# Performance work log

Measured on AMD Instinct MI355X. Metric: run time of the kernel, lower is better.

Reference implementation:

```python
import jax, jax.numpy as jnp
import numpy as np

B, N, C, H = 4, 1024, 768, 12
D = C // H  # head_dim = 64


def setup_inputs() -> dict:
    key = jax.random.key(0)
    ks = jax.random.split(key, 6)
    x = jax.random.normal(ks[0], (B, N, C), dtype=jnp.float32)
    W_qkv = jax.random.normal(ks[1], (C, 3 * C), dtype=jnp.float32) * (C ** -0.5)
    b_qkv = jnp.zeros((3 * C,), dtype=jnp.float32)
    scale = jnp.asarray(D ** -0.5, dtype=jnp.float32)       # learnable scalar in torch
    riem_scale = jnp.asarray(D ** -0.5, dtype=jnp.float32)  # learnable scalar in torch
    # 1x1 Conv2d(2H -> H) == channel-mixing matrix [H, 2H] + bias [H]
    W_conv = jax.random.normal(ks[2], (H, 2 * H), dtype=jnp.float32) * ((2 * H) ** -0.5)
    b_conv = jnp.zeros((H,), dtype=jnp.float32)
    W_proj = jax.random.normal(ks[3], (C, C), dtype=jnp.float32) * (C ** -0.5)
    b_proj = jnp.zeros((C,), dtype=jnp.float32)
    return dict(x=x, W_qkv=W_qkv, b_qkv=b_qkv, scale=scale, riem_scale=riem_scale,
                W_conv=W_conv, b_conv=b_conv, W_proj=W_proj, b_proj=b_proj)


def reference(x, W_qkv, b_qkv, scale, riem_scale, W_conv, b_conv, W_proj, b_proj):
    Bx, Nx, Cx = x.shape
    Hh = W_conv.shape[0]
    d = Cx // Hh
    # qkv projection -> [3, B, H, N, d]
    qkv = (x @ W_qkv + b_qkv).reshape(Bx, Nx, 3, Hh, d).transpose(2, 0, 3, 1, 4)
    q, k, v = qkv[0], qkv[1], qkv[2]
    # standard scaled dot-product scores [B, H, N, N]
    attn = jnp.einsum('bhnd,bhmd->bhnm', q, k) * scale
    # covariance-Frobenius (Riemannian) scores: center along feature dim, then
    # <q_c q_c^T, k_c k_c^T>_F = (q_c . k_c)^2 pairwise
    qc = q - q.mean(axis=-1, keepdims=True)
    kc = k - k.mean(axis=-1, keepdims=True)
    attn_riem = jnp.einsum('bhnd,bhmd->bhnm', qc, kc) ** 2 * riem_scale
    # concat along head/channel dim -> [B, 2H, N, N], then 1x1 conv channel mix
    cat = jnp.concatenate([attn, attn_riem], axis=1)
    mixed = jnp.einsum('bcnm,oc->bonm', cat, W_conv) + b_conv[None, :, None, None]
    attn_ = jax.nn.softmax(mixed, axis=-1)  # [B, H, N, N]
    out = jnp.einsum('bhnm,bhmd->bhnd', attn_, v)
    out = out.transpose(0, 2, 1, 3).reshape(Bx, Nx, Cx)
    return out @ W_proj + b_proj, attn_
```

## Files before the change

### kernel.cpp

```cpp
#include <hip/hip_runtime.h>
#include <cstddef>
#include <cstdint>

#define B_ 4
#define N_ 1024
#define C_ 768
#define H_ 12
#define D_ 64

typedef __attribute__((ext_vector_type(8))) short bf16x8;
typedef __attribute__((ext_vector_type(4))) short s16x4;
typedef __attribute__((ext_vector_type(4))) float f32x4;
typedef __attribute__((ext_vector_type(2))) float f32x2;

#define MFMA16(a_, b_, c_) __builtin_amdgcn_mfma_f32_16x16x32_bf16((a_), (b_), (c_), 0, 0, 0)
#define GLLDS16(gp_, lp_) __builtin_amdgcn_global_load_lds( \
    (const __attribute__((address_space(1))) unsigned int*)(gp_), \
    (__attribute__((address_space(3))) unsigned int*)(lp_), 16, 0, 0)

__device__ __forceinline__ unsigned short f2bf(float f) {
  unsigned int u = __float_as_uint(f);
  u += 0x7fffu + ((u >> 16) & 1u);
  return (unsigned short)(u >> 16);
}
__device__ __forceinline__ float bf2f(unsigned short b) {
  return __uint_as_float(((unsigned int)b) << 16);
}
__device__ __forceinline__ short f2h(float f) {
  _Float16 h = (_Float16)f;
  short s;
  __builtin_memcpy(&s, &h, 2);
  return s;
}
__device__ __forceinline__ float h2f(short s) {
  _Float16 h;
  __builtin_memcpy(&h, &s, 2);
  return (float)h;
}

__global__ __launch_bounds__(256) void k_prep(const float* __restrict__ x,
                                              short* __restrict__ xhi, short* __restrict__ xlo,
                                              const float* __restrict__ Wq,
                                              short* __restrict__ Wthi, short* __restrict__ Wtlo,
                                              const float* __restrict__ Wp,
                                              short* __restrict__ Wpthi, short* __restrict__ Wptlo) {
  __shared__ float tile[32][33];
  const int f = blockIdx.x;
  const int t = threadIdx.x;
  if (f < 1536) {
    const size_t i = ((size_t)f * 256 + t) * 8;
    float4 a = *reinterpret_cast<const float4*>(&x[i]);
    float4 b = *reinterpret_cast<const float4*>(&x[i + 4]);
    float v[8] = {a.x, a.y, a.z, a.w, b.x, b.y, b.z, b.w};
    bf16x8 hi, lo;
#pragma unroll
    for (int j = 0; j < 8; ++j) {
      unsigned short h = f2bf(v[j]);
      hi[j] = (short)h;
      lo[j] = (short)f2bf(v[j] - bf2f(h));
    }
    *reinterpret_cast<bf16x8*>(&xhi[i]) = hi;
    *reinterpret_cast<bf16x8*>(&xlo[i]) = lo;
    return;
  }
  const float* W;
  short *Thi, *Tlo;
  int Kd, Nn, bx, by;
  if (f < 3264) {
    const int local = f - 1536;
    W = Wq; Thi = Wthi; Tlo = Wtlo; Kd = 768; Nn = 2304;
    bx = local % 72; by = local / 72;
  } else {
    const int local = f - 3264;
    W = Wp; Thi = Wpthi; Tlo = Wptlo; Kd = 768; Nn = 768;
    bx = local % 24; by = local / 24;
  }
  const int k0 = by * 32, n0 = bx * 32;
  const int r = t >> 3, cq = (t & 7) * 4;
  float4 v = *reinterpret_cast<const float4*>(&W[(size_t)(k0 + r) * Nn + n0 + cq]);
  tile[r][cq + 0] = v.x; tile[r][cq + 1] = v.y;
  tile[r][cq + 2] = v.z; tile[r][cq + 3] = v.w;
  __syncthreads();
  const int nrow = t >> 3, kq = (t & 7) * 4;
  s16x4 hi, lo;
#pragma unroll
  for (int i = 0; i < 4; ++i) {
    float fv = tile[kq + i][nrow];
    unsigned short h = f2bf(fv);
    hi[i] = (short)h;
    lo[i] = (short)f2bf(fv - bf2f(h));
  }
  *reinterpret_cast<s16x4*>(&Thi[(size_t)(n0 + nrow) * Kd + k0 + kq]) = hi;
  *reinterpret_cast<s16x4*>(&Tlo[(size_t)(n0 + nrow) * Kd + k0 + kq]) = lo;
}

__global__ __launch_bounds__(256) void k_fold(const float* __restrict__ Wc,
                                              const float* __restrict__ scale_p,
                                              const float* __restrict__ riem_p,
                                              float* __restrict__ Wfold) {
  const int t = threadIdx.x;
  const float scale = scale_p[0], riem = riem_p[0];
  for (int i = t; i < 288; i += 256)
    Wfold[i] = Wc[i] * (((i % 24) < 12) ? scale : riem);
}

__global__ __launch_bounds__(256) void k_gemm(const short* __restrict__ Ahi,
                                              const short* __restrict__ Alo,
                                              const short* __restrict__ Bhi,
                                              const short* __restrict__ Blo,
                                              const float* __restrict__ bias,
                                              float* __restrict__ Cout,
                                              int M, int Nn, int Kd) {
  __shared__ __align__(16) short sA[2][128 * 32];
  __shared__ __align__(16) short sB[2][64 * 32];
  const int tid = threadIdx.x;
  const int wv = tid >> 6, l = tid & 63;
  const int lr = l & 15, lg = l >> 4;
  const int row0 = blockIdx.y * 128;
  const int col0 = blockIdx.x * 64;
  const int wr = (wv >> 1) * 64;
  const int wc = (wv & 1) * 32;
  const int ar = tid >> 2, ac = tid & 3;
  f32x4 acc[4][2];
#pragma unroll
  for (int i = 0; i < 4; ++i)
#pragma unroll
    for (int j = 0; j < 2; ++j) acc[i][j] = (f32x4){0.f, 0.f, 0.f, 0.f};

  for (int k0 = 0; k0 < Kd; k0 += 32) {
#pragma unroll
    for (int j = 0; j < 2; ++j) {
      const int row = j * 64 + ar;
      const int cc = ac ^ ((row >> 1) & 3);
      const size_t so = (size_t)(row0 + row) * Kd + k0 + cc * 8;
      GLLDS16(Ahi + so, &sA[0][(j * 256 + (wv << 6)) * 8]);
      GLLDS16(Alo + so, &sA[1][(j * 256 + (wv << 6)) * 8]);
    }
    {
      const int row = ar;
      const int cc = ac ^ ((row >> 1) & 3);
      const size_t so = (size_t)(col0 + row) * Kd + k0 + cc * 8;
      GLLDS16(Bhi + so, &sB[0][(wv << 6) * 8]);
      GLLDS16(Blo + so, &sB[1][(wv << 6) * 8]);
    }
    __syncthreads();
    bf16x8 afh[4], afl[4], bfh[2], bfl[2];
#pragma unroll
    for (int ti = 0; ti < 4; ++ti) {
      const int row = wr + ti * 16 + lr;
      const int pc = lg ^ ((row >> 1) & 3);
      afh[ti] = *reinterpret_cast<const bf16x8*>(&sA[0][row * 32 + pc * 8]);
      afl[ti] = *reinterpret_cast<const bf16x8*>(&sA[1][row * 32 + pc * 8]);
    }
#pragma unroll
    for (int tj = 0; tj < 2; ++tj) {
      const int row = wc + tj * 16 + lr;
      const int pc = lg ^ ((row >> 1) & 3);
      bfh[tj] = *reinterpret_cast<const bf16x8*>(&sB[0][row * 32 + pc * 8]);
      bfl[tj] = *reinterpret_cast<const bf16x8*>(&sB[1][row * 32 + pc * 8]);
    }
#pragma unroll
    for (int ti = 0; ti < 4; ++ti)
#pragma unroll
      for (int tj = 0; tj < 2; ++tj) {
        acc[ti][tj] = MFMA16(afh[ti], bfh[tj], acc[ti][tj]);
        acc[ti][tj] = MFMA16(afl[ti], bfh[tj], acc[ti][tj]);
        acc[ti][tj] = MFMA16(afh[ti], bfl[tj], acc[ti][tj]);
      }
    __syncthreads();
  }
#pragma unroll
  for (int ti = 0; ti < 4; ++ti)
#pragma unroll
    for (int tj = 0; tj < 2; ++tj) {
      const int col = col0 + wc + tj * 16 + lr;
      const float bb = bias[col];
#pragma unroll
      for (int r = 0; r < 4; ++r) {
        const int row = row0 + wr + ti * 16 + lg * 4 + r;
        Cout[(size_t)row * Nn + col] = acc[ti][tj][r] + bb;
      }
    }
}

__global__ __launch_bounds__(256) void k_gemm128(const short* __restrict__ Ahi,
                                                 const short* __restrict__ Alo,
                                                 const short* __restrict__ Bhi,
                                                 const short* __restrict__ Blo,
                                                 const float* __restrict__ bias,
                                                 float* __restrict__ Cout,
                                                 int M, int Nn, int Kd) {
  __shared__ __align__(16) short sA[2][128 * 32];
  __shared__ __align__(16) short sB[2][128 * 32];
  const int tid = threadIdx.x;
  const int wv = tid >> 6, l = tid & 63;
  const int lr = l & 15, lg = l >> 4;
  const int row0 = blockIdx.y * 128;
  const int col0 = blockIdx.x * 128;
  const int wr = (wv >> 1) * 64;
  const int wc = (wv & 1) * 64;
  const int ar = tid >> 2, ac = tid & 3;
  f32x4 acc[4][4];
#pragma unroll
  for (int i = 0; i < 4; ++i)
#pragma unroll
    for (int j = 0; j < 4; ++j) acc[i][j] = (f32x4){0.f, 0.f, 0.f, 0.f};

  for (int k0 = 0; k0 < Kd; k0 += 32) {
#pragma unroll
    for (int j = 0; j < 2; ++j) {
      const int row = j * 64 + ar;
      const int cc = ac ^ ((row >> 1) & 3);
      const size_t ao = (size_t)(row0 + row) * Kd + k0 + cc * 8;
      const size_t bo = (size_t)(col0 + row) * Kd + k0 + cc * 8;
      GLLDS16(Ahi + ao, &sA[0][(j * 256 + (wv << 6)) * 8]);
      GLLDS16(Alo + ao, &sA[1][(j * 256 + (wv << 6)) * 8]);
      GLLDS16(Bhi + bo, &sB[0][(j * 256 + (wv << 6)) * 8]);
      GLLDS16(Blo + bo, &sB[1][(j * 256 + (wv << 6)) * 8]);
    }
    __syncthreads();
    bf16x8 afh[4], afl[4], bfh[4], bfl[4];
#pragma unroll
    for (int ti = 0; ti < 4; ++ti) {
      const int row = wr + ti * 16 + lr;
      const int pc = lg ^ ((row >> 1) & 3);
      afh[ti] = *reinterpret_cast<const bf16x8*>(&sA[0][row * 32 + pc * 8]);
      afl[ti] = *reinterpret_cast<const bf16x8*>(&sA[1][row * 32 + pc * 8]);
    }
#pragma unroll
    for (int tj = 0; tj < 4; ++tj) {
      const int row = wc + tj * 16 + lr;
      const int pc = lg ^ ((row >> 1) & 3);
      bfh[tj] = *reinterpret_cast<const bf16x8*>(&sB[0][row * 32 + pc * 8]);
      bfl[tj] = *reinterpret_cast<const bf16x8*>(&sB[1][row * 32 + pc * 8]);
    }
#pragma unroll
    for (int ti = 0; ti < 4; ++ti)
#pragma unroll
      for (int tj = 0; tj < 4; ++tj) {
        acc[ti][tj] = MFMA16(afh[ti], bfh[tj], acc[ti][tj]);
        acc[ti][tj] = MFMA16(afl[ti], bfh[tj], acc[ti][tj]);
        acc[ti][tj] = MFMA16(afh[ti], bfl[tj], acc[ti][tj]);
      }
    __syncthreads();
  }
#pragma unroll
  for (int ti = 0; ti < 4; ++ti)
#pragma unroll
    for (int tj = 0; tj < 4; ++tj) {
      const int col = col0 + wc + tj * 16 + lr;
      const float bb = bias[col];
#pragma unroll
      for (int r = 0; r < 4; ++r) {
        const int row = row0 + wr + ti * 16 + lg * 4 + r;
        Cout[(size_t)row * Nn + col] = acc[ti][tj][r] + bb;
      }
    }
}

__global__ __launch_bounds__(256) void k_qkv_post(const float* __restrict__ qkvf,
                                                  short* __restrict__ Qhi, short* __restrict__ Qlo,
                                                  short* __restrict__ KChi, short* __restrict__ KClo,
                                                  short* __restrict__ Vt,
                                                  float* __restrict__ Qm, float* __restrict__ Km) {
  __shared__ unsigned short lvh[64][33];
  const int b = blockIdx.z, h = blockIdx.y, n0 = blockIdx.x * 32;
  const int t = threadIdx.x;
  const int row = t >> 3, d0 = (t & 7) * 8;
  const int n = n0 + row;
  const float* base = qkvf + ((size_t)(b * 1024 + n)) * 2304 + h * 64 + d0;
  const size_t qko = ((size_t)(b * H_ + h) * N_ + n) * D_ + d0;

#pragma unroll
  for (int part = 0; part < 2; ++part) {
    float4 a = *reinterpret_cast<const float4*>(base + part * 768);
    float4 c = *reinterpret_cast<const float4*>(base + part * 768 + 4);
    float v[8] = {a.x, a.y, a.z, a.w, c.x, c.y, c.z, c.w};
    float s = v[0] + v[1] + v[2] + v[3] + v[4] + v[5] + v[6] + v[7];
#pragma unroll
    for (int off = 1; off < 8; off <<= 1) s += __shfl_xor(s, off);
    const float mean = s * (1.0f / 64.0f);
    if ((t & 7) == 0) (part ? Km : Qm)[(size_t)(b * H_ + h) * N_ + n] = mean;
    const float sub = part ? mean : 0.0f;
    bf16x8 hi, lo;
#pragma unroll
    for (int j = 0; j < 8; ++j) {
      const float fv = v[j] - sub;
      unsigned short hh = f2bf(fv);
      hi[j] = (short)hh;
      lo[j] = (short)f2bf(fv - bf2f(hh));
    }
    *reinterpret_cast<bf16x8*>((part ? KChi : Qhi) + qko) = hi;
    *reinterpret_cast<bf16x8*>((part ? KClo : Qlo) + qko) = lo;
  }
  {
    float4 a = *reinterpret_cast<const float4*>(base + 1536);
    float4 c = *reinterpret_cast<const float4*>(base + 1536 + 4);
    float v[8] = {a.x, a.y, a.z, a.w, c.x, c.y, c.z, c.w};
#pragma unroll
    for (int j = 0; j < 8; ++j) lvh[d0 + j][row] = f2bf(v[j]);
  }
  __syncthreads();
  const int d = t >> 2, c = t & 3;
  bf16x8 vh;
#pragma unroll
  for (int i = 0; i < 8; ++i) vh[i] = (short)lvh[d][c * 8 + i];
  const size_t vo = ((size_t)(b * H_ + h) * D_ + d) * N_ + n0 + c * 8;
  *reinterpret_cast<bf16x8*>(Vt + vo) = vh;
}

__global__ __launch_bounds__(256, 2) void k_scores(
    const short* __restrict__ Qhi, const short* __restrict__ Qlo,
    const short* __restrict__ KChi, const short* __restrict__ KClo,
    const float* __restrict__ Qm, const float* __restrict__ Km,
    const float* __restrict__ Wfold, float* __restrict__ logits,
    float2* __restrict__ stats) {
  __shared__ __align__(16) short sCh[2][32 * 64];
  __shared__ __align__(16) short sCl[2][32 * 64];
  __shared__ float sQm[12][64];
  __shared__ float sKm[12][32];

  const int t = threadIdx.x;
  const int b = blockIdx.z;
  const int n0 = blockIdx.y * 64, m0 = blockIdx.x * 32;
  const int wv = t >> 6, l = t & 63;
  const int lr = l & 15, lg = l >> 4;
  const size_t bh0 = (size_t)b * H_;

  for (int i = t; i < 768; i += 256)
    sQm[i >> 6][i & 63] = Qm[(bh0 + (i >> 6)) * N_ + n0 + (i & 63)];
  for (int i = t; i < 384; i += 256)
    sKm[i >> 5][i & 31] = Km[(bh0 + (i >> 5)) * N_ + m0 + (i & 31)];

  const int srow = t >> 3;
  const int scs = (t & 7) ^ (srow & 7);
  const size_t csrc = (bh0 * N_ + m0 + srow) * D_ + scs * 8;
  const size_t hstep = (size_t)N_ * D_;
  const int nb = n0 + wv * 16;
  const size_t qsrc = (bh0 * N_ + nb + lr) * D_ + lg * 8;

  GLLDS16(KChi + csrc, &sCh[0][wv * 512]);
  GLLDS16(KClo + csrc, &sCl[0][wv * 512]);
  bf16x8 qh0 = *reinterpret_cast<const bf16x8*>(Qhi + qsrc);
  bf16x8 qh1 = *reinterpret_cast<const bf16x8*>(Qhi + qsrc + 32);
  bf16x8 ql0 = *reinterpret_cast<const bf16x8*>(Qlo + qsrc);
  bf16x8 ql1 = *reinterpret_cast<const bf16x8*>(Qlo + qsrc + 32);

  f32x2 aA01[12], aA23[12], aB01[12], aB23[12];
#pragma unroll
  for (int o = 0; o < 12; ++o) {
    aA01[o] = (f32x2){0.f, 0.f}; aA23[o] = (f32x2){0.f, 0.f};
    aB01[o] = (f32x2){0.f, 0.f}; aB23[o] = (f32x2){0.f, 0.f};
  }

  const int browA = lr, browB = 16 + lr;
  const int aiA0 = browA * 64 + ((lg + 0) ^ (browA & 7)) * 8;
  const int aiA1 = browA * 64 + ((lg + 4) ^ (browA & 7)) * 8;
  const int aiB0 = browB * 64 + ((lg + 0) ^ (browB & 7)) * 8;
  const int aiB1 = browB * 64 + ((lg + 4) ^ (browB & 7)) * 8;
  __syncthreads();

  int buf = 0;
#pragma unroll 2
  for (int h = 0; h < H_; ++h) {
    bf16x8 nqh0, nqh1, nql0, nql1;
    if (h < 11) {
      const size_t cs = csrc + (size_t)(h + 1) * hstep;
      GLLDS16(KChi + cs, &sCh[buf ^ 1][wv * 512]);
      GLLDS16(KClo + cs, &sCl[buf ^ 1][wv * 512]);
      const size_t qs = qsrc + (size_t)(h + 1) * hstep;
      nqh0 = *reinterpret_cast<const bf16x8*>(Qhi + qs);
      nqh1 = *reinterpret_cast<const bf16x8*>(Qhi + qs + 32);
      nql0 = *reinterpret_cast<const bf16x8*>(Qlo + qs);
      nql1 = *reinterpret_cast<const bf16x8*>(Qlo + qs + 32);
    }
    const bf16x8 chA0 = *reinterpret_cast<const bf16x8*>(&sCh[buf][aiA0]);
    const bf16x8 chA1 = *reinterpret_cast<const bf16x8*>(&sCh[buf][aiA1]);
    const bf16x8 clA0 = *reinterpret_cast<const bf16x8*>(&sCl[buf][aiA0]);
    const bf16x8 clA1 = *reinterpret_cast<const bf16x8*>(&sCl[buf][aiA1]);
    const bf16x8 chB0 = *reinterpret_cast<const bf16x8*>(&sCh[buf][aiB0]);
    const bf16x8 chB1 = *reinterpret_cast<const bf16x8*>(&sCh[buf][aiB1]);
    const bf16x8 clB0 = *reinterpret_cast<const bf16x8*>(&sCl[buf][aiB0]);
    const bf16x8 clB1 = *reinterpret_cast<const bf16x8*>(&sCl[buf][aiB1]);

    f32x4 uaA = {0.f, 0.f, 0.f, 0.f}, ubA = {0.f, 0.f, 0.f, 0.f};
    f32x4 uaB = {0.f, 0.f, 0.f, 0.f}, ubB = {0.f, 0.f, 0.f, 0.f};
    uaA = MFMA16(qh0, chA0, uaA);  ubA = MFMA16(qh1, chA1, ubA);
    uaB = MFMA16(qh0, chB0, uaB);  ubB = MFMA16(qh1, chB1, ubB);
    uaA = MFMA16(qh0, clA0, uaA);  ubA = MFMA16(qh1, clA1, ubA);
    uaB = MFMA16(qh0, clB0, uaB);  ubB = MFMA16(qh1, clB1, ubB);
    uaA = MFMA16(ql0, chA0, uaA);  ubA = MFMA16(ql1, chA1, ubA);
    uaB = MFMA16(ql0, chB0, uaB);  ubB = MFMA16(ql1, chB1, ubB);

    const float4 qm4 = *reinterpret_cast<const float4*>(&sQm[h][wv * 16 + lg * 4]);
    const float kmA = 64.0f * sKm[h][lr];
    const float kmB = 64.0f * sKm[h][16 + lr];
    const f32x2 qm01 = {qm4.x, qm4.y};
    const f32x2 qm23 = {qm4.z, qm4.w};
    const f32x2 uA01 = {uaA[0] + ubA[0], uaA[1] + ubA[1]};
    const f32x2 uA23 = {uaA[2] + ubA[2], uaA[3] + ubA[3]};
    const f32x2 uB01 = {uaB[0] + ubB[0], uaB[1] + ubB[1]};
    const f32x2 uB23 = {uaB[2] + ubB[2], uaB[3] + ubB[3]};
    const f32x2 svA01 = kmA * qm01 + uA01;
    const f32x2 svA23 = kmA * qm23 + uA23;
    const f32x2 svB01 = kmB * qm01 + uB01;
    const f32x2 svB23 = kmB * qm23 + uB23;
    const f32x2 u2A01 = uA01 * uA01;
    const f32x2 u2A23 = uA23 * uA23;
    const f32x2 u2B01 = uB01 * uB01;
    const f32x2 u2B23 = uB23 * uB23;
#pragma unroll
    for (int o = 0; o < 12; ++o) {
      const float we = Wfold[o * 24 + h];
      const float wr = Wfold[o * 24 + 12 + h];
      aA01[o] = aA01[o] + we * svA01 + wr * u2A01;
      aA23[o] = aA23[o] + we * svA23 + wr * u2A23;
      aB01[o] = aB01[o] + we * svB01 + wr * u2B01;
      aB23[o] = aB23[o] + we * svB23 + wr * u2B23;
    }
    __syncthreads();
    buf ^= 1;
    if (h < 11) { qh0 = nqh0; qh1 = nqh1; ql0 = nql0; ql1 = nql1; }
  }

#pragma unroll
  for (int o = 0; o < 12; ++o) {
    float avA[4] = {aA01[o][0], aA01[o][1], aA23[o][0], aA23[o][1]};
    float avB[4] = {aB01[o][0], aB01[o][1], aB23[o][0], aB23[o][1]};
    float M4[4], S4[4];
#pragma unroll
    for (int r = 0; r < 4; ++r) {
      float mxA = avA[r], mxB = avB[r];
      mxA = fmaxf(mxA, __shfl_xor(mxA, 1)); mxB = fmaxf(mxB, __shfl_xor(mxB, 1));
      mxA = fmaxf(mxA, __shfl_xor(mxA, 2)); mxB = fmaxf(mxB, __shfl_xor(mxB, 2));
      mxA = fmaxf(mxA, __shfl_xor(mxA, 4)); mxB = fmaxf(mxB, __shfl_xor(mxB, 4));
      mxA = fmaxf(mxA, __shfl_xor(mxA, 8)); mxB = fmaxf(mxB, __shfl_xor(mxB, 8));
      const float M = fmaxf(mxA, mxB);
      float eA = __expf(avA[r] - M);
      float eB = __expf(avB[r] - M);
      float e = eA + eB;
      e += __shfl_xor(e, 1);
      e += __shfl_xor(e, 2);
      e += __shfl_xor(e, 4);
      e += __shfl_xor(e, 8);
      M4[r] = M; S4[r] = e;
    }
#pragma unroll
    for (int r = 0; r < 4; ++r) {
      short* rowp = (short*)(logits + ((bh0 + o) * N_ + nb + lg * 4 + r) * (size_t)N_);
      rowp[m0 + lr] = f2h(avA[r] - M4[r]);
      rowp[m0 + 16 + lr] = f2h(avB[r] - M4[r]);
    }
    if (lr < 4) {
      const int n = nb + lg * 4 + lr;
      stats[(((size_t)b * 12 + o) * 32 + blockIdx.x) * 1024 + n] = make_float2(M4[lr], S4[lr]);
    }
  }
}

__global__ __launch_bounds__(256) void k_pvsm(float* __restrict__ attn,
                                              const float2* __restrict__ stats,
                                              const short* __restrict__ Vt,
                                              short* __restrict__ ohi,
                                              short* __restrict__ olo) {
  __shared__ __align__(16) short sPhi[64 * 64];
  __shared__ __align__(16) short sPlo[64 * 64];
  __shared__ __align__(16) short sV[2][64 * 64];
  __shared__ float sIS[64];
  __shared__ short sMseg16[64 * 32];
  const int flat = blockIdx.x + blockIdx.y * 16 + blockIdx.z * 192;
  const int swz = (flat & 7) * 96 + (flat >> 3);
  const int b = swz / 192;
  const int rem = swz - b * 192;
  const int o = rem >> 4;
  const int n0 = (rem & 15) * 64;
  const int bo = b * H_ + o;
  const int t = threadIdx.x;
  const int wv = t >> 6, l = t & 63;
  const int lr = l & 15, lg = l >> 4;
  const int nsub = wv * 16;

  const int vr0 = t >> 3, vr1 = vr0 + 32;
  const int vc0 = (t & 7) ^ (vr0 & 7);
  const int vc1 = (t & 7) ^ (vr1 & 7);
  const size_t vbase = (size_t)bo * D_ * N_;
  const size_t vs0 = vbase + (size_t)vr0 * N_ + vc0 * 8;
  const size_t vs1 = vbase + (size_t)vr1 * N_ + vc1 * 8;

  GLLDS16(Vt + vs0 + 960, &sV[1][(wv * 64) * 8]);
  GLLDS16(Vt + vs1 + 960, &sV[1][(wv * 64 + 256) * 8]);

  if (t < 64) {
    const int n = n0 + t;
    const float2* sp = stats + ((size_t)bo * 32) * 1024 + n;
    float M = -3.0e38f, S = 0.f;
    for (int seg = 0; seg < 32; ++seg) {
      const float2 p = sp[(size_t)seg * 1024];
      if (p.x > M) {
        S = S * __expf(M - p.x) + p.y;
        M = p.x;
      } else {
        S += p.y * __expf(p.x - M);
      }
    }
    sIS[t] = 1.0f / S;
    for (int seg = 0; seg < 32; ++seg)
      sMseg16[t * 32 + seg] = f2h(sp[(size_t)seg * 1024].x - M);
  }

  const int prow = t >> 3, c0 = (t & 7) * 8;
  float* lrowA = attn + ((size_t)bo * N_ + n0 + prow) * N_;
  float* lrowB = attn + ((size_t)bo * N_ + n0 + prow + 32) * N_;
  const int pofsA = prow * 64 + (((t & 7) ^ (prow & 7)) * 8);
  const int pofsB = pofsA + 32 * 64;

  const int arow = nsub + lr;
  const int ai0 = arow * 64 + (((lg + 0) ^ (arow & 7)) * 8);
  const int ai1 = arow * 64 + (((lg + 4) ^ (arow & 7)) * 8);

  f32x4 acc[4];
#pragma unroll
  for (int dt = 0; dt < 4; ++dt) acc[dt] = (f32x4){0.f, 0.f, 0.f, 0.f};
  __syncthreads();

  for (int mc = 15; mc >= 0; --mc) {
    const int m0 = mc * 64;
    if (mc > 0) {
      const int nb2 = (mc - 1) & 1;
      GLLDS16(Vt + vs0 + m0 - 64, &sV[nb2][(wv * 64) * 8]);
      GLLDS16(Vt + vs1 + m0 - 64, &sV[nb2][(wv * 64 + 256) * 8]);
    }
    const int sidx = mc * 2 + ((t & 7) >> 2);
    const float ofsA = h2f(sMseg16[prow * 32 + sidx]);
    const float ofsB = h2f(sMseg16[(prow + 32) * 32 + sidx]);
    const float iSA = sIS[prow], iSB = sIS[prow + 32];
    const bf16x8 rA = *reinterpret_cast<const bf16x8*>(&((const short*)lrowA)[m0 + c0]);
    const bf16x8 rB = *reinterpret_cast<const bf16x8*>(&((const short*)lrowB)[m0 + c0]);
    float pA[8], pB[8];
#pragma unroll
    for (int j = 0; j < 8; ++j) {
      pA[j] = __expf(h2f(rA[j]) + ofsA) * iSA;
      pB[j] = __expf(h2f(rB[j]) + ofsB) * iSB;
    }
    bf16x8 phiA, ploA, phiB, ploB;
#pragma unroll
    for (int j = 0; j < 8; ++j) {
      unsigned short hA = f2bf(pA[j]);
      phiA[j] = (short)hA;
      ploA[j] = (short)f2bf(pA[j] - bf2f(hA));
      unsigned short hB = f2bf(pB[j]);
      phiB[j] = (short)hB;
      ploB[j] = (short)f2bf(pB[j] - bf2f(hB));
    }
    *reinterpret_cast<bf16x8*>(&sPhi[pofsA]) = phiA;
    *reinterpret_cast<bf16x8*>(&sPlo[pofsA]) = ploA;
    *reinterpret_cast<bf16x8*>(&sPhi[pofsB]) = phiB;
    *reinterpret_cast<bf16x8*>(&sPlo[pofsB]) = ploB;
    __syncthreads();

    float4 oaA = {pA[0], pA[1], pA[2], pA[3]};
    float4 obA = {pA[4], pA[5], pA[6], pA[7]};
    float4 oaB = {pB[0], pB[1], pB[2], pB[3]};
    float4 obB = {pB[4], pB[5], pB[6], pB[7]};
    *reinterpret_cast<float4*>(&lrowA[m0 + c0]) = oaA;
    *reinterpret_cast<float4*>(&lrowA[m0 + c0 + 4]) = obA;
    *reinterpret_cast<float4*>(&lrowB[m0 + c0]) = oaB;
    *reinterpret_cast<float4*>(&lrowB[m0 + c0 + 4]) = obB;

    const int cur = mc & 1;
    const bf16x8 pah0 = *reinterpret_cast<const bf16x8*>(&sPhi[ai0]);
    const bf16x8 pah1 = *reinterpret_cast<const bf16x8*>(&sPhi[ai1]);
    const bf16x8 pal0 = *reinterpret_cast<const bf16x8*>(&sPlo[ai0]);
    const bf16x8 pal1 = *reinterpret_cast<const bf16x8*>(&sPlo[ai1]);
#pragma unroll
    for (int dt = 0; dt < 4; ++dt) {
      const int drow = dt * 16 + lr;
      const bf16x8 vh0 = *reinterpret_cast<const bf16x8*>(&sV[cur][drow * 64 + (((lg + 0) ^ (drow & 7)) * 8)]);
      const bf16x8 vh1 = *reinterpret_cast<const bf16x8*>(&sV[cur][drow * 64 + (((lg + 4) ^ (drow & 7)) * 8)]);
      acc[dt] = MFMA16(pah0, vh0, acc[dt]);
      acc[dt] = MFMA16(pal0, vh0, acc[dt]);
      acc[dt] = MFMA16(pah1, vh1, acc[dt]);
      acc[dt] = MFMA16(pal1, vh1, acc[dt]);
    }
    __syncthreads();
  }
#pragma unroll
  for (int dt = 0; dt < 4; ++dt) {
    const int d = dt * 16 + lr;
#pragma unroll
    for (int r = 0; r < 4; ++r) {
      const int n = n0 + nsub + lg * 4 + r;
      const float val = acc[dt][r];
      const unsigned short hh = f2bf(val);
      const size_t oo = (size_t)(b * 1024 + n) * 768 + o * 64 + d;
      ohi[oo] = (short)hh;
      olo[oo] = (short)f2bf(val - bf2f(hh));
    }
  }
}

extern "C" void kernel_launch(void* const* d_in, const int* in_sizes, int n_in,
                              void* d_out, int out_size, void* d_ws, size_t ws_size,
                              hipStream_t stream) {
  (void)in_sizes; (void)n_in; (void)out_size; (void)ws_size;
  const float* x      = (const float*)d_in[0];
  const float* W_qkv  = (const float*)d_in[1];
  const float* b_qkv  = (const float*)d_in[2];
  const float* scale  = (const float*)d_in[3];
  const float* riem   = (const float*)d_in[4];
  const float* W_conv = (const float*)d_in[5];
  const float* W_proj = (const float*)d_in[7];
  const float* b_proj = (const float*)d_in[8];

  float* out_final = (float*)d_out;
  float* attn_out  = out_final + (size_t)B_ * N_ * C_;

  char* w = (char*)d_ws;
  short* xhi  = (short*)w;
  short* xlo  = xhi + 3145728;
  short* Wthi = (short*)(w + 12582912);
  short* Wtlo = Wthi + 1769472;
  short* Wpthi = (short*)(w + 19660800);
  short* Wptlo = Wpthi + 589824;
  float* qkvf = (float*)(w + 22020096);
  short* Qhi  = (short*)(w + 59768832);
  short* Qlo  = Qhi + 3145728;
  short* KChi = Qlo + 3145728;
  short* KClo = KChi + 3145728;
  short* Vt = xhi;
  float* Wfold = (float*)Wthi;
  float* Qm = (float*)((char*)Wthi + 8192);
  float* Km = (float*)((char*)Wthi + 8192 + 196608);
  float2* stats = (float2*)((char*)qkvf + 12582912);

  short* ohi = Qhi;
  short* olo = Qlo;

  k_prep<<<dim3(3840), 256, 0, stream>>>(x, xhi, xlo, W_qkv, Wthi, Wtlo, W_proj, Wpthi, Wptlo);
  k_gemm128<<<dim3(18, 32), 256, 0, stream>>>(xhi, xlo, Wthi, Wtlo, b_qkv, qkvf, 4096, 2304, 768);
  k_fold<<<dim3(1), 256, 0, stream>>>(W_conv, scale, riem, Wfold);
  k_qkv_post<<<dim3(32, 12, 4), 256, 0, stream>>>(qkvf, Qhi, Qlo, KChi, KClo, Vt, Qm, Km);
  k_scores<<<dim3(32, 16, 4), 256, 0, stream>>>(Qhi, Qlo, KChi, KClo, Qm, Km, Wfold, attn_out, stats);
  k_pvsm<<<dim3(16, 12, 4), 256, 0, stream>>>(attn_out, stats, Vt, ohi, olo);
  k_gemm<<<dim3(12, 32), 256, 0, stream>>>(ohi, olo, Wpthi, Wptlo, b_proj, out_final, 4096, 768, 768);
}
```

Measured before the change: 313.0 us.

## Fuse QKV post-processing into QKV GEMM epilogue and fold k_fold into k_prep

The QKV GEMM epilogue now computes per-row means with shuffles, centers K, splits Q/K into bf16 hi/lo, and transposes V through LDS directly into the final layouts. This removes the fp32 qkv intermediate and the separate k_qkv_post pass. The tiny Wfold computation moves into an extra k_prep block, saving a launch. The price is scattered 2-byte stores for Q/K in the epilogue, which may coalesce poorly, plus a reworked workspace layout.

```diff
diff --git a/kernel.cpp b/kernel.cpp
--- a/kernel.cpp
+++ b/kernel.cpp
@@ -43,10 +43,20 @@
                                               const float* __restrict__ Wq,
                                               short* __restrict__ Wthi, short* __restrict__ Wtlo,
                                               const float* __restrict__ Wp,
-                                              short* __restrict__ Wpthi, short* __restrict__ Wptlo) {
+                                              short* __restrict__ Wpthi, short* __restrict__ Wptlo,
+                                              const float* __restrict__ Wc,
+                                              const float* __restrict__ scale_p,
+                                              const float* __restrict__ riem_p,
+                                              float* __restrict__ Wfold) {
   __shared__ float tile[32][33];
   const int f = blockIdx.x;
   const int t = threadIdx.x;
+  if (f == 3840) {
+    const float scale = scale_p[0], riem = riem_p[0];
+    for (int i = t; i < 288; i += 256)
+      Wfold[i] = Wc[i] * (((i % 24) < 12) ? scale : riem);
+    return;
+  }
   if (f < 1536) {
     const size_t i = ((size_t)f * 256 + t) * 8;
     float4 a = *reinterpret_cast<const float4*>(&x[i]);
@@ -92,16 +102,6 @@
   }
   *reinterpret_cast<s16x4*>(&Thi[(size_t)(n0 + nrow) * Kd + k0 + kq]) = hi;
   *reinterpret_cast<s16x4*>(&Tlo[(size_t)(n0 + nrow) * Kd + k0 + kq]) = lo;
-}
-
-__global__ __launch_bounds__(256) void k_fold(const float* __restrict__ Wc,
-                                              const float* __restrict__ scale_p,
-                                              const float* __restrict__ riem_p,
-                                              float* __restrict__ Wfold) {
-  const int t = threadIdx.x;
-  const float scale = scale_p[0], riem = riem_p[0];
-  for (int i = t; i < 288; i += 256)
-    Wfold[i] = Wc[i] * (((i % 24) < 12) ? scale : riem);
 }
 
 __global__ __launch_bounds__(256) void k_gemm(const short* __restrict__ Ahi,
@@ -183,15 +183,21 @@
     }
 }
 
-__global__ __launch_bounds__(256) void k_gemm128(const short* __restrict__ Ahi,
-                                                 const short* __restrict__ Alo,
-                                                 const short* __restrict__ Bhi,
-                                                 const short* __restrict__ Blo,
-                                                 const float* __restrict__ bias,
-                                                 float* __restrict__ Cout,
-                                                 int M, int Nn, int Kd) {
-  __shared__ __align__(16) short sA[2][128 * 32];
-  __shared__ __align__(16) short sB[2][128 * 32];
+__global__ __launch_bounds__(256) void k_gemm_qkv(const short* __restrict__ Ahi,
+                                                  const short* __restrict__ Alo,
+                                                  const short* __restrict__ Bhi,
+                                                  const short* __restrict__ Blo,
+                                                  const float* __restrict__ bias,
+                                                  short* __restrict__ Qhi, short* __restrict__ Qlo,
+                                                  short* __restrict__ KChi, short* __restrict__ KClo,
+                                                  short* __restrict__ Vt,
+                                                  float* __restrict__ Qm, float* __restrict__ Km) {
+  __shared__ __align__(16) short smem[16384];
+  short* sA0 = smem;
+  short* sA1 = smem + 4096;
+  short* sB0 = smem + 8192;
+  short* sB1 = smem + 12288;
+  const int Kd = 768;
   const int tid = threadIdx.x;
   const int wv = tid >> 6, l = tid & 63;
   const int lr = l & 15, lg = l >> 4;
@@ -213,10 +219,10 @@
       const int cc = ac ^ ((row >> 1) & 3);
       const size_t ao = (size_t)(row0 + row) * Kd + k0 + cc * 8;
       const size_t bo = (size_t)(col0 + row) * Kd + k0 + cc * 8;
-      GLLDS16(Ahi + ao, &sA[0][(j * 256 + (wv << 6)) * 8]);
-      GLLDS16(Alo + ao, &sA[1][(j * 256 + (wv << 6)) * 8]);
-      GLLDS16(Bhi + bo, &sB[0][(j * 256 + (wv << 6)) * 8]);
-      GLLDS16(Blo + bo, &sB[1][(j * 256 + (wv << 6)) * 8]);
+      GLLDS16(Ahi + ao, &sA0[(j * 256 + (wv << 6)) * 8]);
+      GLLDS16(Alo + ao, &sA1[(j * 256 + (wv << 6)) * 8]);
+      GLLDS16(Bhi + bo, &sB0[(j * 256 + (wv << 6)) * 8]);
+      GLLDS16(Blo + bo, &sB1[(j * 256 + (wv << 6)) * 8]);
     }
     __syncthreads();
     bf16x8 afh[4], afl[4], bfh[4], bfl[4];
@@ -224,15 +230,15 @@
     for (int ti = 0; ti < 4; ++ti) {
       const int row = wr + ti * 16 + lr;
       const int pc = lg ^ ((row >> 1) & 3);
-      afh[ti] = *reinterpret_cast<const bf16x8*>(&sA[0][row * 32 + pc * 8]);
-      afl[ti] = *reinterpret_cast<const bf16x8*>(&sA[1][row * 32 + pc * 8]);
+      afh[ti] = *reinterpret_cast<const bf16x8*>(&sA0[row * 32 + pc * 8]);
+      afl[ti] = *reinterpret_cast<const bf16x8*>(&sA1[row * 32 + pc * 8]);
     }
 #pragma unroll
     for (int tj = 0; tj < 4; ++tj) {
       const int row = wc + tj * 16 + lr;
       const int pc = lg ^ ((row >> 1) & 3);
-      bfh[tj] = *reinterpret_cast<const bf16x8*>(&sB[0][row * 32 + pc * 8]);
-      bfl[tj] = *reinterpret_cast<const bf16x8*>(&sB[1][row * 32 + pc * 8]);
+      bfh[tj] = *reinterpret_cast<const bf16x8*>(&sB0[row * 32 + pc * 8]);
+      bfl[tj] = *reinterpret_cast<const bf16x8*>(&sB1[row * 32 + pc * 8]);
     }
 #pragma unroll
     for (int ti = 0; ti < 4; ++ti)
@@ -244,69 +250,72 @@
       }
     __syncthreads();
   }
-#pragma unroll
-  for (int ti = 0; ti < 4; ++ti)
-#pragma unroll
-    for (int tj = 0; tj < 4; ++tj) {
-      const int col = col0 + wc + tj * 16 + lr;
-      const float bb = bias[col];
+
+  const int part = col0 / 768;
+  const int h0 = (col0 - part * 768) >> 6;
+  const int b_ = row0 >> 10;
+  const int nbase = row0 & 1023;
+  const int hh = h0 + (wv & 1);
+  const size_t bh = (size_t)b_ * H_ + hh;
+  float bb[4];
+#pragma unroll
+  for (int tj = 0; tj < 4; ++tj) bb[tj] = bias[col0 + wc + tj * 16 + lr];
+
+  if (part < 2) {
+#pragma unroll
+    for (int ti = 0; ti < 4; ++ti) {
 #pragma unroll
       for (int r = 0; r < 4; ++r) {
-        const int row = row0 + wr + ti * 16 + lg * 4 + r;
-        Cout[(size_t)row * Nn + col] = acc[ti][tj][r] + bb;
+        const int n = nbase + wr + ti * 16 + lg * 4 + r;
+        float v4[4];
+        float s = 0.f;
+#pragma unroll
+        for (int tj = 0; tj < 4; ++tj) {
+          v4[tj] = acc[ti][tj][r] + bb[tj];
+          s += v4[tj];
+        }
+        s += __shfl_xor(s, 1);
+        s += __shfl_xor(s, 2);
+        s += __shfl_xor(s, 4);
+        s += __shfl_xor(s, 8);
+        const float mean = s * (1.0f / 64.0f);
+        const float sub = part ? mean : 0.0f;
+        short* dhi = (part ? KChi : Qhi) + (bh * N_ + n) * D_;
+        short* dlo = (part ? KClo : Qlo) + (bh * N_ + n) * D_;
+#pragma unroll
+        for (int tj = 0; tj < 4; ++tj) {
+          const float fv = v4[tj] - sub;
+          const unsigned short hb = f2bf(fv);
+          const int d = tj * 16 + lr;
+          dhi[d] = (short)hb;
+          dlo[d] = (short)f2bf(fv - bf2f(hb));
+        }
+        if (lr == 0) (part ? Km : Qm)[bh * N_ + n] = mean;
       }
     }
-}
-
-__global__ __launch_bounds__(256) void k_qkv_post(const float* __restrict__ qkvf,
-                                                  short* __restrict__ Qhi, short* __restrict__ Qlo,
-                                                  short* __restrict__ KChi, short* __restrict__ KClo,
-                                                  short* __restrict__ Vt,
-                                                  float* __restrict__ Qm, float* __restrict__ Km) {
-  __shared__ unsigned short lvh[64][33];
-  const int b = blockIdx.z, h = blockIdx.y, n0 = blockIdx.x * 32;
-  const int t = threadIdx.x;
-  const int row = t >> 3, d0 = (t & 7) * 8;
-  const int n = n0 + row;
-  const float* base = qkvf + ((size_t)(b * 1024 + n)) * 2304 + h * 64 + d0;
-  const size_t qko = ((size_t)(b * H_ + h) * N_ + n) * D_ + d0;
-
-#pragma unroll
-  for (int part = 0; part < 2; ++part) {
-    float4 a = *reinterpret_cast<const float4*>(base + part * 768);
-    float4 c = *reinterpret_cast<const float4*>(base + part * 768 + 4);
-    float v[8] = {a.x, a.y, a.z, a.w, c.x, c.y, c.z, c.w};
-    float s = v[0] + v[1] + v[2] + v[3] + v[4] + v[5] + v[6] + v[7];
-#pragma unroll
-    for (int off = 1; off < 8; off <<= 1) s += __shfl_xor(s, off);
-    const float mean = s * (1.0f / 64.0f);
-    if ((t & 7) == 0) (part ? Km : Qm)[(size_t)(b * H_ + h) * N_ + n] = mean;
-    const float sub = part ? mean : 0.0f;
-    bf16x8 hi, lo;
-#pragma unroll
-    for (int j = 0; j < 8; ++j) {
-      const float fv = v[j] - sub;
-      unsigned short hh = f2bf(fv);
-      hi[j] = (short)hh;
-      lo[j] = (short)f2bf(fv - bf2f(hh));
-    }
-    *reinterpret_cast<bf16x8*>((part ? KChi : Qhi) + qko) = hi;
-    *reinterpret_cast<bf16x8*>((part ? KClo : Qlo) + qko) = lo;
-  }
-  {
-    float4 a = *reinterpret_cast<const float4*>(base + 1536);
-    float4 c = *reinterpret_cast<const float4*>(base + 1536 + 4);
-    float v[8] = {a.x, a.y, a.z, a.w, c.x, c.y, c.z, c.w};
-#pragma unroll
-    for (int j = 0; j < 8; ++j) lvh[d0 + j][row] = f2bf(v[j]);
-  }
-  __syncthreads();
-  const int d = t >> 2, c = t & 3;
-  bf16x8 vh;
-#pragma unroll
-  for (int i = 0; i < 8; ++i) vh[i] = (short)lvh[d][c * 8 + i];
-  const size_t vo = ((size_t)(b * H_ + h) * D_ + d) * N_ + n0 + c * 8;
-  *reinterpret_cast<bf16x8*>(Vt + vo) = vh;
+  } else {
+    short* stg = smem + (wv & 1) * 8192;
+#pragma unroll
+    for (int ti = 0; ti < 4; ++ti)
+#pragma unroll
+      for (int r = 0; r < 4; ++r) {
+        const int row = wr + ti * 16 + lg * 4 + r;
+#pragma unroll
+        for (int tj = 0; tj < 4; ++tj) {
+          const int d = tj * 16 + lr;
+          stg[d * 128 + (row ^ ((d & 7) << 3))] = (short)f2bf(acc[ti][tj][r] + bb[tj]);
+        }
+      }
+    __syncthreads();
+    for (int slot = tid; slot < 2048; slot += 256) {
+      const int hd = slot >> 10;
+      const int d = (slot >> 4) & 63;
+      const int c8 = (slot & 15) * 8;
+      bf16x8 vv = *reinterpret_cast<const bf16x8*>(&smem[hd * 8192 + d * 128 + (c8 ^ ((d & 7) << 3))]);
+      const size_t bh2 = (size_t)b_ * H_ + h0 + hd;
+      *reinterpret_cast<bf16x8*>(&Vt[(bh2 * D_ + d) * N_ + nbase + c8]) = vv;
+    }
+  }
 }
 
 __global__ __launch_bounds__(256, 2) void k_scores(
@@ -412,11 +421,11 @@
 #pragma unroll
     for (int o = 0; o < 12; ++o) {
       const float we = Wfold[o * 24 + h];
-      const float wr = Wfold[o * 24 + 12 + h];
-      aA01[o] = aA01[o] + we * svA01 + wr * u2A01;
-      aA23[o] = aA23[o] + we * svA23 + wr * u2A23;
-      aB01[o] = aB01[o] + we * svB01 + wr * u2B01;
-      aB23[o] = aB23[o] + we * svB23 + wr * u2B23;
+      const float wr_ = Wfold[o * 24 + 12 + h];
+      aA01[o] = aA01[o] + we * svA01 + wr_ * u2A01;
+      aA23[o] = aA23[o] + we * svA23 + wr_ * u2A23;
+      aB01[o] = aB01[o] + we * svB01 + wr_ * u2B01;
+      aB23[o] = aB23[o] + we * svB23 + wr_ * u2B23;
     }
     __syncthreads();
     buf ^= 1;
@@ -616,30 +625,28 @@
   float* attn_out  = out_final + (size_t)B_ * N_ * C_;
 
   char* w = (char*)d_ws;
-  short* xhi  = (short*)w;
-  short* xlo  = xhi + 3145728;
-  short* Wthi = (short*)(w + 12582912);
-  short* Wtlo = Wthi + 1769472;
+  short* xhi   = (short*)w;
+  short* xlo   = (short*)(w + 6291456);
+  short* Wthi  = (short*)(w + 12582912);
+  short* Wtlo  = (short*)(w + 16121856);
   short* Wpthi = (short*)(w + 19660800);
-  short* Wptlo = Wpthi + 589824;
-  float* qkvf = (float*)(w + 22020096);
-  short* Qhi  = (short*)(w + 59768832);
-  short* Qlo  = Qhi + 3145728;
-  short* KChi = Qlo + 3145728;
-  short* KClo = KChi + 3145728;
-  short* Vt = xhi;
-  float* Wfold = (float*)Wthi;
-  float* Qm = (float*)((char*)Wthi + 8192);
-  float* Km = (float*)((char*)Wthi + 8192 + 196608);
-  float2* stats = (float2*)((char*)qkvf + 12582912);
-
+  short* Wptlo = (short*)(w + 20840448);
+  short* Qhi   = (short*)(w + 22020096);
+  short* Qlo   = (short*)(w + 28311552);
+  short* KChi  = (short*)(w + 34603008);
+  short* KClo  = (short*)(w + 40894464);
+  short* Vt    = (short*)(w + 47185920);
+  float* Qm    = (float*)(w + 53477376);
+  float* Km    = (float*)(w + 53673984);
+  float* Wfold = (float*)(w + 53870592);
+  float2* stats = (float2*)(w + 53874688);
   short* ohi = Qhi;
   short* olo = Qlo;
 
-  k_prep<<<dim3(3840), 256, 0, stream>>>(x, xhi, xlo, W_qkv, Wthi, Wtlo, W_proj, Wpthi, Wptlo);
-  k_gemm128<<<dim3(18, 32), 256, 0, stream>>>(xhi, xlo, Wthi, Wtlo, b_qkv, qkvf, 4096, 2304, 768);
-  k_fold<<<dim3(1), 256, 0, stream>>>(W_conv, scale, riem, Wfold);
-  k_qkv_post<<<dim3(32, 12, 4), 256, 0, stream>>>(qkvf, Qhi, Qlo, KChi, KClo, Vt, Qm, Km);
+  k_prep<<<dim3(3841), 256, 0, stream>>>(x, xhi, xlo, W_qkv, Wthi, Wtlo, W_proj, Wpthi, Wptlo,
+                                         W_conv, scale, riem, Wfold);
+  k_gemm_qkv<<<dim3(18, 32), 256, 0, stream>>>(xhi, xlo, Wthi, Wtlo, b_qkv,
+                                               Qhi, Qlo, KChi, KClo, Vt, Qm, Km);
   k_scores<<<dim3(32, 16, 4), 256, 0, stream>>>(Qhi, Qlo, KChi, KClo, Qm, Km, Wfold, attn_out, stats);
   k_pvsm<<<dim3(16, 12, 4), 256, 0, stream>>>(attn_out, stats, Vt, ohi, olo);
   k_gemm<<<dim3(12, 32), 256, 0, stream>>>(ohi, olo, Wpthi, Wptlo, b_proj, out_final, 4096, 768, 768);
```

After: 299.3 us (median of 2 runs). 4.4% less time.
